# Kernel tuning notes

Measured on AMD Instinct MI355X. Metric: run time of the kernel, lower is better.

Reference implementation:

```python
import jax, jax.numpy as jnp
import numpy as np

MIN_NORM = 1e-15
PROJ_EPS = 4e-3


def _artanh(x):
    x = jnp.clip(x, -1 + 1e-7, 1 - 1e-7)
    return 0.5 * (jnp.log1p(x) - jnp.log1p(-x))


def _norm(x):
    return jnp.clip(jnp.linalg.norm(x, axis=-1, keepdims=True), MIN_NORM)


def proj(x, c):
    norm = _norm(x)
    maxnorm = (1.0 - PROJ_EPS) / jnp.sqrt(c)
    return jnp.where(norm > maxnorm, x / norm * maxnorm, x)


def expmap0(u, c):
    sqrt_c = jnp.sqrt(c)
    u_norm = _norm(u)
    return jnp.tanh(sqrt_c * u_norm) * u / (sqrt_c * u_norm)


def logmap0(p, c):
    sqrt_c = jnp.sqrt(c)
    p_norm = _norm(p)
    return _artanh(sqrt_c * p_norm) * p / (sqrt_c * p_norm)


def mobius_add(x, y, c):
    x2 = jnp.sum(x * x, axis=-1, keepdims=True)
    y2 = jnp.sum(y * y, axis=-1, keepdims=True)
    xy = jnp.sum(x * y, axis=-1, keepdims=True)
    num = (1 + 2 * c * xy + c * y2) * x + (1 - c * x2) * y
    denom = 1 + 2 * c * xy + c * c * x2 * y2
    return num / jnp.clip(denom, MIN_NORM)


def mobius_matvec(m, x, c):
    sqrt_c = jnp.sqrt(c)
    x_norm = _norm(x)
    mx = x @ m.T
    mx_norm = _norm(mx)
    res = jnp.tanh(mx_norm / x_norm * _artanh(sqrt_c * x_norm)) * mx / (mx_norm * sqrt_c)
    zero_row = jnp.all(mx == 0, axis=-1, keepdims=True)
    return jnp.where(zero_row, jnp.zeros_like(res), res)


def setup_inputs() -> dict:
    key = jax.random.key(0)
    k1, k2, k3, k4, k5 = jax.random.split(key, 5)
    n, d, e = 50000, 128, 800000
    c = jnp.float32(1.0)
    x = 0.1 * jax.random.normal(k1, (n, d), dtype=jnp.float32)
    x = proj(x, c)  # points on the Poincare ball
    adj = jax.random.randint(k2, (2, e), 0, n, dtype=jnp.int64)
    w = jax.random.uniform(k3, (e,), dtype=jnp.float32)
    weight = jax.random.normal(k4, (d, d), dtype=jnp.float32) * (1.0 / np.sqrt(d))
    bias = jax.random.normal(k5, (d,), dtype=jnp.float32) * 0.01
    return {"x": x, "adj": adj, "w": w, "weight": weight, "bias": bias}


def reference(x, adj, w, weight, bias):
    c_in = jnp.float32(1.0)
    c_out = jnp.float32(1.0)
    n = x.shape[0]

    # HypLinear (dropout p=0 -> identity on weight)
    mv = mobius_matvec(weight, x, c_in)
    res = proj(mv, c_in)
    b = bias.reshape(1, -1)  # proj_tan0 is identity on the Poincare ball
    hyp_bias = proj(expmap0(b, c_in), c_in)
    h = proj(mobius_add(res, hyp_bias, c_in), c_in)

    # HypAgg: logmap0 -> weighted segment_sum over edges -> expmap0 -> proj
    s, r = adj[0], adj[1]
    ht = logmap0(h, c_in)
    x_s = ht[s] * w[:, None]  # [E, d]
    x_agg = jax.ops.segment_sum(x_s, r, num_segments=n)
    h = proj(expmap0(x_agg, c_in), c_in)

    # HypAct: act(logmap0) -> expmap0 -> proj
    xt = jax.nn.relu(logmap0(h, c_in))
    out = proj(expmap0(xt, c_out), c_out)
    return (out, adj)
```

## Files before the change

kernel.cpp:

```cpp
#include <hip/hip_runtime.h>
#include <math.h>

#define MAXN 0.996f
#define MINN 1e-15f
#define CAPQ 1536

typedef __bf16   bf16x8  __attribute__((ext_vector_type(8)));
typedef _Float16 halfx8  __attribute__((ext_vector_type(8)));
typedef _Float16 half2_t __attribute__((ext_vector_type(2)));
typedef float    floatx4 __attribute__((ext_vector_type(4)));

__device__ __forceinline__ float wsum(float v){
  v += __shfl_xor(v, 32);
  v += __shfl_xor(v, 16);
  v += __shfl_xor(v, 8);
  v += __shfl_xor(v, 4);
  v += __shfl_xor(v, 2);
  v += __shfl_xor(v, 1);
  return v;
}

__device__ __forceinline__ float artanh_(float v){
  v = fminf(fmaxf(v, -1.f + 1e-7f), 1.f - 1e-7f);
  return 0.5f * (log1pf(v) - log1pf(-v));
}

__device__ __forceinline__ int block_excl_scan(int v, int tid, int* wsums){
  int lane = tid & 63, wid = tid >> 6;
  int iv = v;
#pragma unroll
  for(int o = 1; o < 64; o <<= 1){
    int t = __shfl_up(iv, o);
    if(lane >= o) iv += t;
  }
  if(lane == 63) wsums[wid] = iv;
  __syncthreads();
  int wbase = 0;
  for(int k = 0; k < wid; k++) wbase += wsums[k];
  return wbase + iv - v;
}

__global__ __launch_bounds__(256)
void fusedA_kernel(const float* __restrict__ x, const float* __restrict__ W,
                   const float* __restrict__ bias, _Float16* __restrict__ ht, int n,
                   const int* __restrict__ adj, const float* __restrict__ w,
                   float* __restrict__ adj_out, int* __restrict__ bucketSize,
                   int2* __restrict__ part, int E, int nA)
{
  __shared__ __align__(16) char smem[49408];
  const int tid = threadIdx.x;

  if(blockIdx.x < nA){
    int* hist  = (int*)smem;
    int* cur   = (int*)(smem + 4096);
    int* lbase = (int*)(smem + 8192);
    int* gbase = (int*)(smem + 12288);
    int* wsA   = (int*)(smem + 16384);
    int2* stag = (int2*)(smem + 16400);

#pragma unroll
    for(int k = 0; k < 4; k++) hist[k*256 + tid] = 0;
    __syncthreads();

    const int e0 = blockIdx.x * 4096;
    int p0r[16], p1r[16];
#pragma unroll
    for(int k = 0; k < 16; k++){
      int e = e0 + k*256 + tid;
      if(e < E){
        int s = adj[e];
        int r = adj[e + E];
        float we = w[e];
        adj_out[e]     = (float)s;
        adj_out[e + E] = (float)r;
        int bin = r >> 6;
        p0r[k] = s | ((r & 63) << 16) | (bin << 22);
        p1r[k] = __float_as_int(we);
        atomicAdd(&hist[bin], 1);
      }
    }
    __syncthreads();
    int c0 = hist[4*tid], c1 = hist[4*tid+1], c2 = hist[4*tid+2], c3 = hist[4*tid+3];
    int cb = c0 + c1 + c2 + c3;
    int lb = block_excl_scan(cb, tid, wsA);
    int l0 = lb, l1 = lb + c0, l2 = l1 + c1, l3 = l2 + c2;
    lbase[4*tid] = l0; lbase[4*tid+1] = l1; lbase[4*tid+2] = l2; lbase[4*tid+3] = l3;
    cur[4*tid]   = l0; cur[4*tid+1]   = l1; cur[4*tid+2]   = l2; cur[4*tid+3]   = l3;
    gbase[4*tid]   = c0 ? atomicAdd(&bucketSize[4*tid],   c0) : 0;
    gbase[4*tid+1] = c1 ? atomicAdd(&bucketSize[4*tid+1], c1) : 0;
    gbase[4*tid+2] = c2 ? atomicAdd(&bucketSize[4*tid+2], c2) : 0;
    gbase[4*tid+3] = c3 ? atomicAdd(&bucketSize[4*tid+3], c3) : 0;
    __syncthreads();
#pragma unroll
    for(int k = 0; k < 16; k++){
      int e = e0 + k*256 + tid;
      if(e < E){
        int bin = ((unsigned)p0r[k]) >> 22;
        int pos = atomicAdd(&cur[bin], 1);
        stag[pos] = make_int2(p0r[k], p1r[k]);
      }
    }
    __syncthreads();
    int total = (e0 + 4096 <= E) ? 4096 : (E - e0);
    for(int i = tid; i < total; i += 256){
      int2 p = stag[i];
      int bin = ((unsigned)p.x) >> 22;
      int loc = gbase[bin] + (i - lbase[bin]);
      if(loc < CAPQ) part[(size_t)bin * CAPQ + loc] = p;
    }
    return;
  }

  __bf16* Wh   = (__bf16*)smem;
  float* hb_sh = (float*)(smem + 32768);
  float* y2_sh = (float*)(smem + 33280);

  for(int g = tid; g < 2048; g += 256){
    int nr = g >> 4, k16 = g & 15;
    const float* wp = W + nr * 128 + k16 * 8;
    float4 a = *(const float4*)wp;
    float4 b = *(const float4*)(wp + 4);
    bf16x8 h;
    h[0]=(__bf16)a.x; h[1]=(__bf16)a.y; h[2]=(__bf16)a.z; h[3]=(__bf16)a.w;
    h[4]=(__bf16)b.x; h[5]=(__bf16)b.y; h[6]=(__bf16)b.z; h[7]=(__bf16)b.w;
    *(bf16x8*)&Wh[nr * 128 + ((k16 ^ (nr & 15)) << 3)] = h;
  }
  if(tid < 64){
    int l = tid;
    float b0 = bias[l], b1 = bias[l + 64];
    float bn = fmaxf(sqrtf(wsum(b0*b0 + b1*b1)), MINN);
    float sb = tanhf(bn) / bn;
    float hb0 = sb*b0, hb1 = sb*b1;
    float hnn = fmaxf(sqrtf(wsum(hb0*hb0 + hb1*hb1)), MINN);
    if(hnn > MAXN){ float f = MAXN/hnn; hb0 *= f; hb1 *= f; }
    float y2 = wsum(hb0*hb0 + hb1*hb1);
    hb_sh[l] = hb0; hb_sh[l + 64] = hb1;
    if(l == 0) *y2_sh = y2;
  }
  __syncthreads();

  const int lane = tid & 63;
  const int wid  = tid >> 6;
  const int q    = lane >> 4;
  const int n15  = lane & 15;

  const int M0 = (blockIdx.x - nA) * 64 + wid * 16;
  if(M0 >= n) return;

  float hbv[8];
#pragma unroll
  for(int t = 0; t < 8; t++) hbv[t] = hb_sh[t*16 + n15];
  const float y2 = *y2_sh;

  floatx4 acc[8];
#pragma unroll
  for(int t = 0; t < 8; t++) acc[t] = (floatx4){0.f,0.f,0.f,0.f};

  float x2p = 0.f;
  int m = M0 + n15; if(m > n - 1) m = n - 1;
#pragma unroll
  for(int kk = 0; kk < 4; kk++){
    const float* xp = x + (size_t)m * 128 + kk * 32 + q * 8;
    float4 xa = *(const float4*)xp;
    float4 xb = *(const float4*)(xp + 4);
    x2p += xa.x*xa.x + xa.y*xa.y + xa.z*xa.z + xa.w*xa.w
         + xb.x*xb.x + xb.y*xb.y + xb.z*xb.z + xb.w*xb.w;
    bf16x8 a;
    a[0]=(__bf16)xa.x; a[1]=(__bf16)xa.y; a[2]=(__bf16)xa.z; a[3]=(__bf16)xa.w;
    a[4]=(__bf16)xb.x; a[5]=(__bf16)xb.y; a[6]=(__bf16)xb.z; a[7]=(__bf16)xb.w;
    int k16 = kk * 4 + q;
#pragma unroll
    for(int t = 0; t < 8; t++){
      bf16x8 b = *(bf16x8*)&Wh[(t*16 + n15) * 128 + ((k16 ^ n15) << 3)];
      acc[t] = __builtin_amdgcn_mfma_f32_16x16x32_bf16(a, b, acc[t], 0, 0, 0);
    }
  }
  x2p += __shfl_xor(x2p, 16);
  x2p += __shfl_xor(x2p, 32);

  float mp[4], dp[4];
#pragma unroll
  for(int i = 0; i < 4; i++){
    float mpi = 0.f, dpi = 0.f;
#pragma unroll
    for(int t = 0; t < 8; t++){ float v = acc[t][i]; mpi = fmaf(v, v, mpi); dpi = fmaf(v, hbv[t], dpi); }
    mpi += __shfl_xor(mpi, 1); mpi += __shfl_xor(mpi, 2); mpi += __shfl_xor(mpi, 4); mpi += __shfl_xor(mpi, 8);
    dpi += __shfl_xor(dpi, 1); dpi += __shfl_xor(dpi, 2); dpi += __shfl_xor(dpi, 4); dpi += __shfl_xor(dpi, 8);
    mp[i] = mpi; dp[i] = dpi;
  }

  const int li   = lane & 3;
  const int srcl = (((lane >> 2) << 4) | li) & 63;
  float selmp = li==0 ? mp[0] : li==1 ? mp[1] : li==2 ? mp[2] : mp[3];
  float seldp = li==0 ? dp[0] : li==1 ? dp[1] : li==2 ? dp[2] : dp[3];
  float tmp_mp = __shfl(selmp, srcl);
  float tmp_dp = __shfl(seldp, srcl);
  float mxn = fmaxf(sqrtf(tmp_mp), MINN);
  float xn  = fmaxf(sqrtf(x2p), MINN);
  float tt  = tanhf(mxn / xn * artanh_(xn));
  float s1  = tt / mxn;
  float rn  = fmaxf(tt, MINN);
  if(rn > MAXN) s1 *= MAXN / rn;
  float xy    = s1 * tmp_dp;
  float r2    = s1 * s1 * tmp_mp;
  float alpha = 1.f + 2.f*xy + y2;
  float beta  = 1.f - r2;
  float inv   = 1.f / fmaxf(1.f + 2.f*xy + r2*y2, MINN);
  float as1   = alpha * s1;

  float as1b[4], betab[4], invb[4];
#pragma unroll
  for(int i = 0; i < 4; i++){
    int sl = ((lane >> 4) << 2) | i;
    as1b[i]  = __shfl(as1, sl);
    betab[i] = __shfl(beta, sl);
    invb[i]  = __shfl(inv, sl);
  }

  float uv[4][8];
  float u2[4];
#pragma unroll
  for(int i = 0; i < 4; i++){
    float u2i = 0.f;
#pragma unroll
    for(int t = 0; t < 8; t++){
      float u = (as1b[i] * acc[t][i] + betab[i] * hbv[t]) * invb[i];
      uv[i][t] = u;
      u2i = fmaf(u, u, u2i);
    }
    u2i += __shfl_xor(u2i, 1); u2i += __shfl_xor(u2i, 2); u2i += __shfl_xor(u2i, 4); u2i += __shfl_xor(u2i, 8);
    u2[i] = u2i;
  }

  float selu = li==0 ? u2[0] : li==1 ? u2[1] : li==2 ? u2[2] : u2[3];
  float tu   = __shfl(selu, srcl);
  float un = fmaxf(sqrtf(tu), MINN);
  float sc = 1.f, hn = un;
  if(un > MAXN){ sc = MAXN/un; hn = MAXN; }
  float lt = artanh_(hn) / hn * sc;

#pragma unroll
  for(int i = 0; i < 4; i++){
    int grow = M0 + q * 4 + i;
    float lti = __shfl(lt, ((lane >> 4) << 2) | i);
    if(grow < n){
      halfx8 f;
#pragma unroll
      for(int t = 0; t < 8; t++) f[t] = (_Float16)(lti * uv[i][t]);
      *(halfx8*)(ht + (size_t)grow * 128 + n15 * 8) = f;
    }
  }
}

__global__ __launch_bounds__(1024)
void aggB_kernel(const int* __restrict__ bucketSize, const int2* __restrict__ part,
                 const _Float16* __restrict__ ht, float* __restrict__ out, int n)
{
  __shared__ unsigned epk_l[CAPQ];
  __shared__ int hist[64];
  __shared__ int rowoff[65];
  __shared__ int cursor[64];
  __shared__ float tr[16][4][132];

  const int tid = threadIdx.x;
  const int b   = blockIdx.x;

  if(tid < 64) hist[tid] = 0;
  __syncthreads();

  int size = bucketSize[b]; if(size > CAPQ) size = CAPQ;
  const int2* src = part + (size_t)b * CAPQ;
  int2 e0v, e1v;
  const bool v0 = tid < size;
  const bool v1 = tid + 1024 < size;
  if(v0) e0v = src[tid];
  if(v1) e1v = src[tid + 1024];
  if(v0) atomicAdd(&hist[(((unsigned)e0v.x) >> 16) & 63], 1);
  if(v1) atomicAdd(&hist[(((unsigned)e1v.x) >> 16) & 63], 1);
  __syncthreads();
  if(tid < 64){
    int v = hist[tid];
    int iv = v;
#pragma unroll
    for(int o = 1; o < 64; o <<= 1){ int t = __shfl_up(iv, o); if(tid >= o) iv += t; }
    rowoff[tid + 1] = iv;
    cursor[tid]     = iv - v;
    if(tid == 0) rowoff[0] = 0;
  }
  __syncthreads();
#define PUTE(ev) { \
    int rl = (((unsigned)ev.x) >> 16) & 63; \
    int p = atomicAdd(&cursor[rl], 1); \
    unsigned wh = (unsigned)__builtin_bit_cast(unsigned short, \
                    (_Float16)__builtin_bit_cast(float, ev.y)); \
    epk_l[p] = (unsigned)(ev.x & 0xFFFF) | (wh << 16); }
  if(v0) PUTE(e0v);
  if(v1) PUTE(e1v);
#undef PUTE
  __syncthreads();

  const int gi   = tid >> 4;
  const int i    = tid & 15;
  const int wid  = tid >> 6;
  const int g    = (tid >> 4) & 3;
  const int row  = b * 64 + gi;
  const char* htb = (const char*)ht;
  const int ioff = i << 4;

  half2_t acc2[4];
#pragma unroll
  for(int k = 0; k < 4; k++) acc2[k] = (half2_t){(_Float16)0.f, (_Float16)0.f};

#define EDGE(pk) { \
    int s_ = (int)((pk) & 0xFFFFu); \
    half2_t w2_ = __builtin_bit_cast(half2_t, __builtin_amdgcn_perm(pk, pk, 0x03020302u)); \
    int4 q_ = *(const int4*)(htb + ((s_ << 8) | ioff)); \
    acc2[0] = __builtin_bit_cast(half2_t, q_.x) * w2_ + acc2[0]; \
    acc2[1] = __builtin_bit_cast(half2_t, q_.y) * w2_ + acc2[1]; \
    acc2[2] = __builtin_bit_cast(half2_t, q_.z) * w2_ + acc2[2]; \
    acc2[3] = __builtin_bit_cast(half2_t, q_.w) * w2_ + acc2[3]; \
  }

  if(row < n){
    int beg = rowoff[gi];
    int m   = rowoff[gi + 1] - beg;
    const unsigned* ep = epk_l + beg;
    int t = 0;
    for(; t + 3 < m; t += 4){
      unsigned pk0 = ep[t], pk1 = ep[t+1], pk2 = ep[t+2], pk3 = ep[t+3];
      EDGE(pk0); EDGE(pk1); EDGE(pk2); EDGE(pk3);
    }
    for(; t + 1 < m; t += 2){
      unsigned pk0 = ep[t], pk1 = ep[t+1];
      EDGE(pk0); EDGE(pk1);
    }
    if(t < m){ unsigned pk0 = ep[t]; EDGE(pk0); }
  }
#undef EDGE

  float acc[8];
#pragma unroll
  for(int k = 0; k < 4; k++){
    acc[2*k]   = (float)acc2[k][0];
    acc[2*k+1] = (float)acc2[k][1];
  }
  float u2p = 0.f;
#pragma unroll
  for(int k = 0; k < 8; k++) u2p = fmaf(acc[k], acc[k], u2p);
  u2p += __shfl_xor(u2p, 1); u2p += __shfl_xor(u2p, 2);
  u2p += __shfl_xor(u2p, 4); u2p += __shfl_xor(u2p, 8);
  float un = fmaxf(sqrtf(u2p), MINN);
  float te = tanhf(un);
  float se = te / un;
  float gn = fmaxf(te, MINN);
  float hn = gn;
  if(gn > MAXN){ se *= MAXN/gn; hn = MAXN; }
  float la = artanh_(hn) / hn * se;
  float l[8];
  float r2p = 0.f;
#pragma unroll
  for(int k = 0; k < 8; k++){ l[k] = fmaxf(la*acc[k], 0.f); r2p = fmaf(l[k], l[k], r2p); }
  r2p += __shfl_xor(r2p, 1); r2p += __shfl_xor(r2p, 2);
  r2p += __shfl_xor(r2p, 4); r2p += __shfl_xor(r2p, 8);
  float rn = fmaxf(sqrtf(r2p), MINN);
  float t2 = tanhf(rn);
  float s2 = t2 / rn;
  float on = fmaxf(t2, MINN);
  if(on > MAXN) s2 *= MAXN/on;

  if(row < n){
#pragma unroll
    for(int k = 0; k < 8; k++) tr[wid][g][k*16 + i] = s2 * l[k];
    float4 o0 = *(float4*)&tr[wid][g][i*8];
    float4 o1 = *(float4*)&tr[wid][g][i*8 + 4];
    float* orow = out + (size_t)row * 128 + i*8;
    *(float4*)orow       = o0;
    *(float4*)(orow + 4) = o1;
  }
}

extern "C" void kernel_launch(void* const* d_in, const int* in_sizes, int n_in,
                              void* d_out, int out_size, void* d_ws, size_t ws_size,
                              hipStream_t stream)
{
  const float* x    = (const float*)d_in[0];
  const int*   adj  = (const int*)  d_in[1];
  const float* w    = (const float*)d_in[2];
  const float* W    = (const float*)d_in[3];
  const float* bias = (const float*)d_in[4];
  const int n = in_sizes[0] / 128;
  const int E = in_sizes[2];

  float* out     = (float*)d_out;
  float* adj_out = out + (size_t)n * 128;

  char* ws = (char*)d_ws;
  _Float16* ht   = (_Float16*)ws;  ws += (size_t)n * 128 * sizeof(_Float16);
  int2*  part    = (int2*)ws;      ws += (size_t)1024 * CAPQ * sizeof(int2);
  int*   bucketSize = (int*)ws;

  const int nA = (E + 4095) / 4096;
  const int nS = (n + 63) / 64;
  const int nB = (n + 63) / 64;

  hipMemsetAsync(bucketSize, 0, 1024 * sizeof(int), stream);
  fusedA_kernel<<<nA + nS, 256, 0, stream>>>(x, W, bias, ht, n,
                                             adj, w, adj_out, bucketSize, part, E, nA);
  aggB_kernel<<<nB, 1024, 0, stream>>>(bucketSize, part, ht, out, n);
}
```

Measured before the change: 148.2 us.

## Scatter edges directly to global buckets and compute hyperbolic bias per wavefront

The edge-partition blocks no longer do a block-local scan and stage records in shared memory for an ordered write-out. Each edge now claims its global bucket slot through a shared-memory atomic counter seeded from the global bucket atomic and writes straight to global memory. The GEMM blocks compute the hyperbolic bias redundantly in every wavefront with shuffles instead of sharing it through LDS. Together these cut the shared-memory footprint from about 48 KB to 32 KB, which may allow more resident blocks, and remove a barrier and the scan. The cost is scattered, less coalesced global writes and order within a bucket that is no longer deterministic.

```diff
diff --git a/kernel.cpp b/kernel.cpp
--- a/kernel.cpp
+++ b/kernel.cpp
@@ -25,21 +25,6 @@
   return 0.5f * (log1pf(v) - log1pf(-v));
 }
 
-__device__ __forceinline__ int block_excl_scan(int v, int tid, int* wsums){
-  int lane = tid & 63, wid = tid >> 6;
-  int iv = v;
-#pragma unroll
-  for(int o = 1; o < 64; o <<= 1){
-    int t = __shfl_up(iv, o);
-    if(lane >= o) iv += t;
-  }
-  if(lane == 63) wsums[wid] = iv;
-  __syncthreads();
-  int wbase = 0;
-  for(int k = 0; k < wid; k++) wbase += wsums[k];
-  return wbase + iv - v;
-}
-
 __global__ __launch_bounds__(256)
 void fusedA_kernel(const float* __restrict__ x, const float* __restrict__ W,
                    const float* __restrict__ bias, _Float16* __restrict__ ht, int n,
@@ -47,16 +32,12 @@
                    float* __restrict__ adj_out, int* __restrict__ bucketSize,
                    int2* __restrict__ part, int E, int nA)
 {
-  __shared__ __align__(16) char smem[49408];
+  __shared__ __align__(16) char smem[32768];
   const int tid = threadIdx.x;
 
   if(blockIdx.x < nA){
-    int* hist  = (int*)smem;
-    int* cur   = (int*)(smem + 4096);
-    int* lbase = (int*)(smem + 8192);
-    int* gbase = (int*)(smem + 12288);
-    int* wsA   = (int*)(smem + 16384);
-    int2* stag = (int2*)(smem + 16400);
+    int* hist = (int*)smem;
+    int* cur  = (int*)(smem + 4096);
 
 #pragma unroll
     for(int k = 0; k < 4; k++) hist[k*256 + tid] = 0;
@@ -80,16 +61,12 @@
       }
     }
     __syncthreads();
-    int c0 = hist[4*tid], c1 = hist[4*tid+1], c2 = hist[4*tid+2], c3 = hist[4*tid+3];
-    int cb = c0 + c1 + c2 + c3;
-    int lb = block_excl_scan(cb, tid, wsA);
-    int l0 = lb, l1 = lb + c0, l2 = l1 + c1, l3 = l2 + c2;
-    lbase[4*tid] = l0; lbase[4*tid+1] = l1; lbase[4*tid+2] = l2; lbase[4*tid+3] = l3;
-    cur[4*tid]   = l0; cur[4*tid+1]   = l1; cur[4*tid+2]   = l2; cur[4*tid+3]   = l3;
-    gbase[4*tid]   = c0 ? atomicAdd(&bucketSize[4*tid],   c0) : 0;
-    gbase[4*tid+1] = c1 ? atomicAdd(&bucketSize[4*tid+1], c1) : 0;
-    gbase[4*tid+2] = c2 ? atomicAdd(&bucketSize[4*tid+2], c2) : 0;
-    gbase[4*tid+3] = c3 ? atomicAdd(&bucketSize[4*tid+3], c3) : 0;
+#pragma unroll
+    for(int k = 0; k < 4; k++){
+      int bin = k*256 + tid;
+      int c = hist[bin];
+      cur[bin] = c ? atomicAdd(&bucketSize[bin], c) : 0;
+    }
     __syncthreads();
 #pragma unroll
     for(int k = 0; k < 16; k++){
@@ -97,23 +74,13 @@
       if(e < E){
         int bin = ((unsigned)p0r[k]) >> 22;
         int pos = atomicAdd(&cur[bin], 1);
-        stag[pos] = make_int2(p0r[k], p1r[k]);
+        if(pos < CAPQ) part[(size_t)bin * CAPQ + pos] = make_int2(p0r[k], p1r[k]);
       }
     }
-    __syncthreads();
-    int total = (e0 + 4096 <= E) ? 4096 : (E - e0);
-    for(int i = tid; i < total; i += 256){
-      int2 p = stag[i];
-      int bin = ((unsigned)p.x) >> 22;
-      int loc = gbase[bin] + (i - lbase[bin]);
-      if(loc < CAPQ) part[(size_t)bin * CAPQ + loc] = p;
-    }
     return;
   }
 
-  __bf16* Wh   = (__bf16*)smem;
-  float* hb_sh = (float*)(smem + 32768);
-  float* y2_sh = (float*)(smem + 33280);
+  __bf16* Wh = (__bf16*)smem;
 
   for(int g = tid; g < 2048; g += 256){
     int nr = g >> 4, k16 = g & 15;
@@ -125,32 +92,29 @@
     h[4]=(__bf16)b.x; h[5]=(__bf16)b.y; h[6]=(__bf16)b.z; h[7]=(__bf16)b.w;
     *(bf16x8*)&Wh[nr * 128 + ((k16 ^ (nr & 15)) << 3)] = h;
   }
-  if(tid < 64){
-    int l = tid;
-    float b0 = bias[l], b1 = bias[l + 64];
-    float bn = fmaxf(sqrtf(wsum(b0*b0 + b1*b1)), MINN);
-    float sb = tanhf(bn) / bn;
-    float hb0 = sb*b0, hb1 = sb*b1;
-    float hnn = fmaxf(sqrtf(wsum(hb0*hb0 + hb1*hb1)), MINN);
-    if(hnn > MAXN){ float f = MAXN/hnn; hb0 *= f; hb1 *= f; }
-    float y2 = wsum(hb0*hb0 + hb1*hb1);
-    hb_sh[l] = hb0; hb_sh[l + 64] = hb1;
-    if(l == 0) *y2_sh = y2;
-  }
-  __syncthreads();
 
   const int lane = tid & 63;
   const int wid  = tid >> 6;
   const int q    = lane >> 4;
   const int n15  = lane & 15;
 
+  float b0 = bias[lane], b1 = bias[lane + 64];
+  float bn = fmaxf(sqrtf(wsum(b0*b0 + b1*b1)), MINN);
+  float sb = tanhf(bn) / bn;
+  float hb0 = sb*b0, hb1 = sb*b1;
+  float hnn = fmaxf(sqrtf(wsum(hb0*hb0 + hb1*hb1)), MINN);
+  if(hnn > MAXN){ float f = MAXN/hnn; hb0 *= f; hb1 *= f; }
+  const float y2 = wsum(hb0*hb0 + hb1*hb1);
+  float hbv[8];
+#pragma unroll
+  for(int t = 0; t < 4; t++) hbv[t]     = __shfl(hb0, t*16 + n15);
+#pragma unroll
+  for(int t = 0; t < 4; t++) hbv[t + 4] = __shfl(hb1, t*16 + n15);
+
+  __syncthreads();
+
   const int M0 = (blockIdx.x - nA) * 64 + wid * 16;
   if(M0 >= n) return;
-
-  float hbv[8];
-#pragma unroll
-  for(int t = 0; t < 8; t++) hbv[t] = hb_sh[t*16 + n15];
-  const float y2 = *y2_sh;
 
   floatx4 acc[8];
 #pragma unroll
```

Result: faster. 134.3 us (-9.4%).
